# Optimization experiments

Hardware: AMD Instinct MI355X
Metric: run time of the kernel (lower is better)

## Reference

```python
import jax, jax.numpy as jnp
import numpy as np

B, S, DIM = 2, 2048, 2048
N_HEADS = 16
KV_LORA = 512
NOPE_D = 128
ROPE_D = 64
V_D = 128
Q_D = NOPE_D + ROPE_D  # 192
EPS = 1e-6


def _make_rope_cache(seqlen, head_dim):
    # [cos | sin] layout per position, GPT-NeoX half-rotation convention
    half = head_dim // 2
    inv_freq = 1.0 / (10000.0 ** (np.arange(0, half, dtype=np.float32) / half))
    t = np.arange(seqlen, dtype=np.float32)
    freqs = np.outer(t, inv_freq)                    # [S, half]
    emb = np.concatenate([freqs, freqs], axis=-1)    # [S, head_dim]
    return jnp.asarray(np.concatenate([np.cos(emb), np.sin(emb)], axis=-1))  # [S, 2*head_dim]


def setup_inputs() -> dict:
    key = jax.random.key(0)
    ks = jax.random.split(key, 6)
    x = jax.random.normal(ks[0], (B, S, DIM), dtype=jnp.float32)
    rope_cache = _make_rope_cache(S, ROPE_D)         # [S, 128]
    std = 0.02
    wq = jax.random.normal(ks[1], (N_HEADS * Q_D, DIM), dtype=jnp.float32) * std
    wkva = jax.random.normal(ks[2], (KV_LORA + ROPE_D, DIM), dtype=jnp.float32) * std
    norm_w = jnp.ones((KV_LORA,), dtype=jnp.float32)
    wkvb = jax.random.normal(ks[3], (N_HEADS * (NOPE_D + V_D), KV_LORA), dtype=jnp.float32) * std
    wo = jax.random.normal(ks[4], (DIM, N_HEADS * V_D), dtype=jnp.float32) * std
    return {"x": x, "rope_cache": rope_cache, "wq": wq, "wkva": wkva,
            "norm_w": norm_w, "wkvb": wkvb, "wo": wo}


def _rotate_half(t):
    h = t.shape[-1] // 2
    return jnp.concatenate([-t[..., h:], t[..., :h]], axis=-1)


def _rms_norm(t, w):
    tf = t.astype(jnp.float32)
    y = tf * jax.lax.rsqrt(jnp.mean(tf * tf, axis=-1, keepdims=True) + EPS)
    return (y * w).astype(t.dtype)


def reference(x, rope_cache, wq, wkva, norm_w, wkvb, wo):
    bs, seqlen, _ = x.shape
    scale = Q_D ** (-0.5)

    q = (x @ wq.T).reshape(bs, seqlen, N_HEADS, Q_D)
    q_nope, q_rope = q[..., :NOPE_D], q[..., NOPE_D:]

    ckv = x @ wkva.T                                 # [b,s,KV_LORA+ROPE_D]
    kv_pass, k_rope = ckv[..., :KV_LORA], ckv[..., KV_LORA:]
    kv = (_rms_norm(kv_pass, norm_w) @ wkvb.T).reshape(bs, seqlen, N_HEADS, NOPE_D + V_D)
    k_nope, v = kv[..., :NOPE_D], kv[..., NOPE_D:]

    k_rope = jnp.broadcast_to(k_rope[:, :, None, :], (bs, seqlen, N_HEADS, ROPE_D))

    cos = rope_cache[:seqlen, :ROPE_D][None, :, None, :]
    sin = rope_cache[:seqlen, ROPE_D:2 * ROPE_D][None, :, None, :]
    q_rope = q_rope * cos + _rotate_half(q_rope) * sin
    k_rope = k_rope * cos + _rotate_half(k_rope) * sin

    qf = jnp.concatenate([q_nope, q_rope], axis=-1)  # [b,s,h,192]
    kf = jnp.concatenate([k_nope, k_rope], axis=-1)

    # causal SDPA
    scores = jnp.einsum('bqhd,bkhd->bhqk', qf, kf) * scale
    mask = jnp.tril(jnp.ones((seqlen, seqlen), dtype=bool))
    scores = jnp.where(mask, scores, jnp.finfo(scores.dtype).min)
    probs = jax.nn.softmax(scores, axis=-1)
    out = jnp.einsum('bhqk,bkhd->bqhd', probs, v).reshape(bs, seqlen, N_HEADS * V_D)
    return out @ wo.T
```

## Files before the change

kernel.cpp:

```cpp
#include <hip/hip_runtime.h>
#include <cstdint>
#include <cstddef>

#define B_      2
#define S_      2048
#define DIM_    2048
#define H_      16
#define KV_LORA_ 512
#define NOPE_D_ 128
#define ROPE_D_ 64
#define V_D_    128
#define Q_D_    192
#define EPS_    1e-6f
#define BS_     (B_ * S_)
#define CKV_P_  768

typedef __attribute__((ext_vector_type(8))) short bf16x8;
typedef __attribute__((ext_vector_type(4))) float f32x4;
typedef __attribute__((ext_vector_type(16))) float f32x16;

__device__ __forceinline__ ushort f2bf(float f) {
    union { float f; uint32_t u; } v; v.f = f;
    uint32_t u = v.u + 0x7fff + ((v.u >> 16) & 1);
    return (ushort)(u >> 16);
}
__device__ __forceinline__ float bf2f(ushort u) {
    union { uint32_t u; float f; } v; v.u = (uint32_t)u << 16; return v.f;
}
__device__ __forceinline__ void gll16(const void* g, void* l) {
    __builtin_amdgcn_global_load_lds(
        (const __attribute__((address_space(1))) unsigned int*)g,
        (__attribute__((address_space(3))) unsigned int*)l, 16, 0, 0);
}

#define GQ_BARRIER()  __builtin_amdgcn_s_barrier()
#define GQ_LGKM0()    do { asm volatile("s_waitcnt lgkmcnt(0)" ::: "memory"); \
                           __builtin_amdgcn_sched_barrier(0); } while (0)

template <int MODE>
__global__ __launch_bounds__(512, 2) void gemm256_8ph(
    const ushort* __restrict__ A, const ushort* __restrict__ Bw,
    void* __restrict__ Cv, void* __restrict__ Cv2, int N, int K, int nbx)
{
    __shared__ __align__(16) ushort L[2][2][2][8192];

    const int tid = threadIdx.x;
    const int lane = tid & 63;
    const int w = tid >> 6;
    const int l15 = lane & 15, quad = lane >> 4;
    const int q8 = quad * 8;
    const int rsw8 = ((l15 >> 1) & 3) * 8;

    const int nwg = (int)gridDim.x;
    const int cpx = nwg >> 3;
    const int lin = (int)blockIdx.x;
    const int swz = (lin & 7) * cpx + (lin >> 3);
    const int m0 = (swz / nbx) * 256;
    const int n0 = (swz % nbx) * 256;

    const int wm0 = (w & 3) * 64;
    const int wn0 = (w >> 2) * 128;

    const int NT = K >> 6;

    f32x4 acc[4][8];
#pragma unroll
    for (int i = 0; i < 4; ++i)
#pragma unroll
        for (int j = 0; j < 8; ++j) acc[i][j] = (f32x4){0.f, 0.f, 0.f, 0.f};

    const int srow = lane >> 2;
    const int scg  = (lane & 3) ^ ((lane >> 3) & 3);

    auto stage = [&](int ab, int kh, int kt, int buf) {
#pragma unroll
        for (int j = 0; j < 2; ++j) {
            int ci = w + j * 8;
            ushort* dst = &L[buf][ab][kh][ci * 512 + lane * 8];
            int row = ci * 16 + srow;
            const ushort* src = (ab ? Bw + (size_t)(n0 + row) * K
                                    : A  + (size_t)(m0 + row) * K)
                                + kt * 64 + kh * 32 + scg * 8;
            gll16(src, dst);
        }
    };

    stage(0, 0, 0, 0); stage(1, 0, 0, 0); stage(0, 1, 0, 0); stage(1, 1, 0, 0);
    if (NT > 1) { stage(0, 0, 1, 1); stage(1, 0, 1, 1); stage(0, 1, 1, 1); }
    else        { stage(0, 0, 0, 1); stage(1, 0, 0, 1); stage(0, 1, 0, 1); }
    asm volatile("s_waitcnt vmcnt(6)" ::: "memory");
    GQ_BARRIER();

    bf16x8 a[4], b[4];

    for (int t = 0; t < NT; ++t) {
        const int c = t & 1, o = c ^ 1;
        const int kt1 = (t + 1 < NT) ? t + 1 : 0;
        const int kt2 = (t + 2 < NT) ? t + 2 : 0;

#pragma unroll
        for (int fm = 0; fm < 4; ++fm)
            a[fm] = *(const bf16x8*)&L[c][0][0][(wm0 + fm * 16 + l15) * 32 + (q8 ^ rsw8)];
#pragma unroll
        for (int fn = 0; fn < 4; ++fn)
            b[fn] = *(const bf16x8*)&L[c][1][0][(wn0 + fn * 16 + l15) * 32 + (q8 ^ rsw8)];
        stage(1, 1, kt1, o);
        GQ_BARRIER();
        GQ_LGKM0();
        __builtin_amdgcn_s_setprio(1);
#pragma unroll
        for (int fm = 0; fm < 4; ++fm)
#pragma unroll
            for (int fn = 0; fn < 4; ++fn)
                acc[fm][fn] = __builtin_amdgcn_mfma_f32_16x16x32_bf16(a[fm], b[fn], acc[fm][fn], 0, 0, 0);
        __builtin_amdgcn_s_setprio(0);
        GQ_BARRIER();

#pragma unroll
        for (int fn = 0; fn < 4; ++fn)
            b[fn] = *(const bf16x8*)&L[c][1][0][(wn0 + 64 + fn * 16 + l15) * 32 + (q8 ^ rsw8)];
        stage(0, 0, kt2, c);
        GQ_BARRIER();
        GQ_LGKM0();
        __builtin_amdgcn_s_setprio(1);
#pragma unroll
        for (int fm = 0; fm < 4; ++fm)
#pragma unroll
            for (int fn = 0; fn < 4; ++fn)
                acc[fm][4 + fn] = __builtin_amdgcn_mfma_f32_16x16x32_bf16(a[fm], b[fn], acc[fm][4 + fn], 0, 0, 0);
        __builtin_amdgcn_s_setprio(0);
        GQ_BARRIER();

#pragma unroll
        for (int fm = 0; fm < 4; ++fm)
            a[fm] = *(const bf16x8*)&L[c][0][1][(wm0 + fm * 16 + l15) * 32 + (q8 ^ rsw8)];
#pragma unroll
        for (int fn = 0; fn < 4; ++fn)
            b[fn] = *(const bf16x8*)&L[c][1][1][(wn0 + fn * 16 + l15) * 32 + (q8 ^ rsw8)];
        stage(1, 0, kt2, c);
        GQ_BARRIER();
        GQ_LGKM0();
        __builtin_amdgcn_s_setprio(1);
#pragma unroll
        for (int fm = 0; fm < 4; ++fm)
#pragma unroll
            for (int fn = 0; fn < 4; ++fn)
                acc[fm][fn] = __builtin_amdgcn_mfma_f32_16x16x32_bf16(a[fm], b[fn], acc[fm][fn], 0, 0, 0);
        __builtin_amdgcn_s_setprio(0);
        GQ_BARRIER();

#pragma unroll
        for (int fn = 0; fn < 4; ++fn)
            b[fn] = *(const bf16x8*)&L[c][1][1][(wn0 + 64 + fn * 16 + l15) * 32 + (q8 ^ rsw8)];
        stage(0, 1, kt2, c);
        GQ_BARRIER();
        GQ_LGKM0();
        __builtin_amdgcn_s_setprio(1);
#pragma unroll
        for (int fm = 0; fm < 4; ++fm)
#pragma unroll
            for (int fn = 0; fn < 4; ++fn)
                acc[fm][4 + fn] = __builtin_amdgcn_mfma_f32_16x16x32_bf16(a[fm], b[fn], acc[fm][4 + fn], 0, 0, 0);
        __builtin_amdgcn_s_setprio(0);
        asm volatile("s_waitcnt vmcnt(6)" ::: "memory");
        GQ_BARRIER();
    }

    if (MODE == 3) {
        asm volatile("s_waitcnt vmcnt(0)" ::: "memory");
        GQ_BARRIER();
        const int h = n0 >> 8;
        if (w < 4) {
#pragma unroll
            for (int fm = 0; fm < 4; ++fm)
#pragma unroll
                for (int r = 0; r < 4; ++r) {
                    size_t base = (size_t)(m0 + wm0 + fm * 16 + quad * 4 + r) * 4096
                                  + n0 + wn0 + l15;
#pragma unroll
                    for (int fn = 0; fn < 8; ++fn)
                        ((ushort*)Cv)[base + fn * 16] = f2bf(acc[fm][fn][r]);
                }
        } else {
            ushort* T = &L[0][0][0][0] + (size_t)(w - 4) * (128 * 80);
#pragma unroll
            for (int fm = 0; fm < 4; ++fm)
#pragma unroll
                for (int fn = 0; fn < 8; ++fn) {
                    uint32_t lo = (uint32_t)f2bf(acc[fm][fn][0])
                                | ((uint32_t)f2bf(acc[fm][fn][1]) << 16);
                    uint32_t hi2 = (uint32_t)f2bf(acc[fm][fn][2])
                                 | ((uint32_t)f2bf(acc[fm][fn][3]) << 16);
                    uint2 pk; pk.x = lo; pk.y = hi2;
                    *(uint2*)&T[(size_t)(fn * 16 + l15) * 80 + fm * 16 + quad * 4] = pk;
                }
            asm volatile("s_waitcnt lgkmcnt(0)" ::: "memory");
            __builtin_amdgcn_sched_barrier(0);
            const int bh = (m0 >> 11) * 16 + h;
            const int sbase = (m0 & 2047) + (w & 3) * 64;
            ushort* vT = (ushort*)Cv2;
#pragma unroll
            for (int j = 0; j < 16; ++j) {
                int cc = j * 64 + lane;
                int vd = cc >> 3;
                int s8 = (cc & 7) * 8;
                bf16x8 v = *(const bf16x8*)&T[(size_t)vd * 80 + s8];
                *(bf16x8*)(vT + ((size_t)bh * 128 + vd) * 2048 + sbase + s8) = v;
            }
        }
        return;
    }
#pragma unroll
    for (int fm = 0; fm < 4; ++fm)
#pragma unroll
        for (int r = 0; r < 4; ++r) {
            int row = m0 + wm0 + fm * 16 + quad * 4 + r;
            if (MODE == 2) {
                if (n0 < 3072) {
                    size_t base = (size_t)row * 3072 + n0 + wn0 + l15;
#pragma unroll
                    for (int fn = 0; fn < 8; ++fn)
                        ((ushort*)Cv)[base + fn * 16] = f2bf(acc[fm][fn][r]);
                } else {
                    size_t base = (size_t)row * CKV_P_ + (n0 - 3072) + wn0 + l15;
#pragma unroll
                    for (int fn = 0; fn < 8; ++fn)
                        ((float*)Cv2)[base + fn * 16] = acc[fm][fn][r];
                }
            } else {
                size_t base = (size_t)row * N + n0 + wn0 + l15;
#pragma unroll
                for (int fn = 0; fn < 8; ++fn) {
                    float v = acc[fm][fn][r];
                    if (MODE == 1) ((ushort*)Cv)[base + fn * 16] = f2bf(v);
                    else           ((float*)Cv)[base + fn * 16] = v;
                }
            }
        }
}

template <int OUT_BF16>
__global__ __launch_bounds__(512, 2) void gemm_bn128(
    const ushort* __restrict__ A, const ushort* __restrict__ Bw,
    void* __restrict__ Cv, int N, int K, int nbx)
{
    __shared__ __align__(16) ushort LA[2][2][4][256][8];
    __shared__ __align__(16) ushort LB[2][2][4][128][8];

    const int tid = threadIdx.x;
    const int lane = tid & 63;
    const int w = tid >> 6;
    const int l15 = lane & 15, quad = lane >> 4;

    const int nwg = (int)gridDim.x;
    const int cpx = nwg >> 3;
    const int lin = (int)blockIdx.x;
    const int swz = (lin & 7) * cpx + (lin >> 3);
    const int m0 = (swz / nbx) * 256;
    const int n0 = (swz % nbx) * 128;

    const int wm0 = (w & 3) * 64;
    const int wn0 = (w >> 2) * 64;

    const int NT = K >> 6;

    f32x4 acc[4][4];
#pragma unroll
    for (int i = 0; i < 4; ++i)
#pragma unroll
        for (int j = 0; j < 4; ++j) acc[i][j] = (f32x4){0.f, 0.f, 0.f, 0.f};

    auto stageA = [&](int kh, int kt, int buf) {
#pragma unroll
        for (int j = 0; j < 2; ++j) {
            int ci = w + j * 8;
            int qd = ci >> 2, rg = ci & 3;
            ushort* dst = &LA[buf][kh][qd][rg * 64 + lane][0];
            const ushort* src = A + (size_t)(m0 + rg * 64 + lane) * K
                                + kt * 64 + kh * 32 + qd * 8;
            gll16(src, dst);
        }
    };
    auto stageB = [&](int kt, int buf) {
#pragma unroll
        for (int j = 0; j < 2; ++j) {
            int ci = w + j * 8;
            int kh = ci >> 3, qd = (ci >> 1) & 3, rh = ci & 1;
            ushort* dst = &LB[buf][kh][qd][rh * 64 + lane][0];
            const ushort* src = Bw + (size_t)(n0 + rh * 64 + lane) * K
                                + kt * 64 + kh * 32 + qd * 8;
            gll16(src, dst);
        }
    };

    stageA(0, 0, 0); stageA(1, 0, 0); stageB(0, 0);
    stageA(0, (NT > 1) ? 1 : 0, 1);
    asm volatile("s_waitcnt vmcnt(2)" ::: "memory");
    GQ_BARRIER();

    bf16x8 a[4], b[4];

    for (int t = 0; t < NT; ++t) {
        const int c = t & 1, o = c ^ 1;
        const int kt1 = (t + 1 < NT) ? t + 1 : 0;
        const int kt2 = (t + 2 < NT) ? t + 2 : 0;

#pragma unroll
        for (int fm = 0; fm < 4; ++fm)
            a[fm] = *(const bf16x8*)&LA[c][0][quad][wm0 + fm * 16 + l15][0];
#pragma unroll
        for (int fn = 0; fn < 4; ++fn)
            b[fn] = *(const bf16x8*)&LB[c][0][quad][wn0 + fn * 16 + l15][0];
        stageA(1, kt1, o); stageB(kt1, o);
        GQ_BARRIER();
        GQ_LGKM0();
        __builtin_amdgcn_s_setprio(1);
#pragma unroll
        for (int fm = 0; fm < 4; ++fm)
#pragma unroll
            for (int fn = 0; fn < 4; ++fn)
                acc[fm][fn] = __builtin_amdgcn_mfma_f32_16x16x32_bf16(a[fm], b[fn], acc[fm][fn], 0, 0, 0);
        __builtin_amdgcn_s_setprio(0);
        GQ_BARRIER();

#pragma unroll
        for (int fm = 0; fm < 4; ++fm)
            a[fm] = *(const bf16x8*)&LA[c][1][quad][wm0 + fm * 16 + l15][0];
#pragma unroll
        for (int fn = 0; fn < 4; ++fn)
            b[fn] = *(const bf16x8*)&LB[c][1][quad][wn0 + fn * 16 + l15][0];
        stageA(0, kt2, c);
        GQ_BARRIER();
        GQ_LGKM0();
        __builtin_amdgcn_s_setprio(1);
#pragma unroll
        for (int fm = 0; fm < 4; ++fm)
#pragma unroll
            for (int fn = 0; fn < 4; ++fn)
                acc[fm][fn] = __builtin_amdgcn_mfma_f32_16x16x32_bf16(a[fm], b[fn], acc[fm][fn], 0, 0, 0);
        __builtin_amdgcn_s_setprio(0);
        asm volatile("s_waitcnt vmcnt(2)" ::: "memory");
        GQ_BARRIER();
    }

#pragma unroll
    for (int fm = 0; fm < 4; ++fm)
#pragma unroll
        for (int r = 0; r < 4; ++r) {
            size_t base = (size_t)(m0 + wm0 + fm * 16 + quad * 4 + r) * N + n0 + wn0 + l15;
#pragma unroll
            for (int fn = 0; fn < 4; ++fn) {
                float v = acc[fm][fn][r];
                if (OUT_BF16) ((ushort*)Cv)[base + fn * 16] = f2bf(v);
                else          ((float*)Cv)[base + fn * 16] = v;
            }
        }
}

__global__ __launch_bounds__(256) void cast_all(
    const float* __restrict__ x, const float* __restrict__ wq,
    const float* __restrict__ wkva, const float* __restrict__ wkvb,
    const float* __restrict__ wo,
    ushort* __restrict__ xb, ushort* __restrict__ wc,
    ushort* __restrict__ wkvb_bf, ushort* __restrict__ wo_bf)
{
    size_t i = ((size_t)blockIdx.x * 256 + threadIdx.x) * 8;
    const float* s; ushort* d;
    if (i < 8388608)        { s = x + i;                  d = xb + i; }
    else if (i < 14680064)  { s = wq + (i - 8388608);     d = wc + (i - 8388608); }
    else if (i < 15859712)  { s = wkva + (i - 14680064);  d = wc + (i - 8388608); }
    else if (i < 16252928)  {
        ushort4 z = {0, 0, 0, 0};
        ushort* dz = wc + (i - 8388608);
        *(ushort4*)dz = z; *(ushort4*)(dz + 4) = z;
        return;
    }
    else if (i < 18350080)  { s = wkvb + (i - 16252928);  d = wkvb_bf + (i - 16252928); }
    else                    { s = wo + (i - 18350080);    d = wo_bf + (i - 18350080); }
    float4 a = *(const float4*)s;
    float4 b = *(const float4*)(s + 4);
    ushort4 o0, o1;
    o0.x = f2bf(a.x); o0.y = f2bf(a.y); o0.z = f2bf(a.z); o0.w = f2bf(a.w);
    o1.x = f2bf(b.x); o1.y = f2bf(b.y); o1.z = f2bf(b.z); o1.w = f2bf(b.w);
    *(ushort4*)d = o0;
    *(ushort4*)(d + 4) = o1;
}

__global__ __launch_bounds__(256) void rmsnorm_rope_k(
    const float* __restrict__ ckv, const float* __restrict__ nw,
    const float* __restrict__ rope_cache,
    ushort* __restrict__ cnorm, ushort* __restrict__ krb)
{
    const int lane = threadIdx.x & 63;
    const int row = blockIdx.x * 4 + (threadIdx.x >> 6);
    const float* src = ckv + (size_t)row * CKV_P_;
    float4 a = *(const float4*)(src + lane * 4);
    float4 b = *(const float4*)(src + 256 + lane * 4);
    float ss = a.x*a.x + a.y*a.y + a.z*a.z + a.w*a.w
             + b.x*b.x + b.y*b.y + b.z*b.z + b.w*b.w;
#pragma unroll
    for (int off = 32; off > 0; off >>= 1) ss += __shfl_xor(ss, off, 64);
    float rs = rsqrtf(ss * (1.0f / 512.0f) + EPS_);
    float4 w0 = *(const float4*)(nw + lane * 4);
    float4 w1 = *(const float4*)(nw + 256 + lane * 4);
    ushort* dst = cnorm + (size_t)row * KV_LORA_;
    ushort4 o0, o1;
    o0.x = f2bf(a.x*rs*w0.x); o0.y = f2bf(a.y*rs*w0.y);
    o0.z = f2bf(a.z*rs*w0.z); o0.w = f2bf(a.w*rs*w0.w);
    o1.x = f2bf(b.x*rs*w1.x); o1.y = f2bf(b.y*rs*w1.y);
    o1.z = f2bf(b.z*rs*w1.z); o1.w = f2bf(b.w*rs*w1.w);
    *(ushort4*)(dst + lane * 4) = o0;
    *(ushort4*)(dst + 256 + lane * 4) = o1;

    float v = src[KV_LORA_ + lane];
    float other = __shfl_xor(v, 32, 64);
    float rot = (lane < 32) ? -other : other;
    int s = row & (S_ - 1);
    float c  = rope_cache[s * (2 * ROPE_D_) + lane];
    float sn = rope_cache[s * (2 * ROPE_D_) + ROPE_D_ + lane];
    krb[(size_t)row * ROPE_D_ + lane] = f2bf(v * c + rot * sn);
}

__global__ __launch_bounds__(512, 2) void mla_attn_mfma6(
    const ushort* __restrict__ qb, const ushort* __restrict__ kvb,
    const ushort* __restrict__ krb, const ushort* __restrict__ vT,
    const float* __restrict__ rope_cache, ushort* __restrict__ attn)
{
    __shared__ __align__(16) ushort LDSU[40960];
    const int KFo[2] = {0, 12288};
    const int VFo[2] = {24576, 32768};

    const int tid = threadIdx.x;
    const int lane = tid & 63;
    const int w = tid >> 6;
    const int l31 = lane & 31, hi = lane >> 5;
    const int band = w & 3;
    const int koff = (w >> 2) * 32;

    const int lin = (int)blockIdx.y * 8 + (int)blockIdx.x;
    const int swz = (lin & 7) * 32 + (lin >> 3);
    const int bh = swz >> 3;
    const int px = swz & 7;
    const int b = bh >> 4, h = bh & 15;
    const size_t bS = (size_t)b * S_;
    const float scale = 0.07216878364870323f;

    auto stage = [&](int kbase, int bufi) {
#pragma unroll
        for (int r = 0; r < 3; ++r) {
            int c = w + r * 8;
            ushort* dst = &LDSU[KFo[bufi] + (c * 64 + lane) * 8];
            const ushort* src = (c < 16)
                ? kvb + (bS + kbase + lane) * 4096 + h * 256 + c * 8
                : krb + (bS + kbase + lane) * 64 + (c - 16) * 8;
            gll16(src, dst);
        }
#pragma unroll
        for (int r = 0; r < 2; ++r) {
            int c = w + r * 8;
            ushort* dst = &LDSU[VFo[bufi] + (((c & 7) * 128) + (c >> 3) * 64 + lane) * 8];
            const ushort* src =
                vT + ((size_t)bh * 128 + (c >> 3) * 64 + lane) * S_ + kbase + (c & 7) * 8;
            gll16(src, dst);
        }
    };

#pragma unroll 1
    for (int hv = 0; hv < 2; ++hv) {
        const int qt = hv ? 15 - px : px;
        const int qbase = qt * 128;
        const int nkt = 2 * qt + 2;
        const int bmin = qbase + band * 32;

        stage(0, 0);

        bf16x8 qf[12];
        {
            const ushort* qrow = qb + (bS + bmin + l31) * (size_t)(H_ * Q_D_) + h * Q_D_;
#pragma unroll
            for (int c = 0; c < 8; ++c)
                qf[c] = *(const bf16x8*)(qrow + c * 16 + hi * 8);
            bf16x8 q8  = *(const bf16x8*)(qrow + 128 + hi * 8);
            bf16x8 q9  = *(const bf16x8*)(qrow + 144 + hi * 8);
            bf16x8 q10 = *(const bf16x8*)(qrow + 160 + hi * 8);
            bf16x8 q11 = *(const bf16x8*)(qrow + 176 + hi * 8);
            const float* rc = rope_cache + (size_t)(bmin + l31) * 128 + hi * 8;
            f32x4 c8a = *(const f32x4*)(rc + 0),  c8b = *(const f32x4*)(rc + 4);
            f32x4 c9a = *(const f32x4*)(rc + 16), c9b = *(const f32x4*)(rc + 20);
            f32x4 cAa = *(const f32x4*)(rc + 32), cAb = *(const f32x4*)(rc + 36);
            f32x4 cBa = *(const f32x4*)(rc + 48), cBb = *(const f32x4*)(rc + 52);
            f32x4 s8a = *(const f32x4*)(rc + 64), s8b = *(const f32x4*)(rc + 68);
            f32x4 s9a = *(const f32x4*)(rc + 80), s9b = *(const f32x4*)(rc + 84);
            f32x4 sAa = *(const f32x4*)(rc + 96), sAb = *(const f32x4*)(rc + 100);
            f32x4 sBa = *(const f32x4*)(rc + 112), sBb = *(const f32x4*)(rc + 116);
            bf16x8 o8, o9, o10, o11;
#pragma unroll
            for (int e = 0; e < 4; ++e) {
                float a8 = bf2f((ushort)q8[e]),  b8 = bf2f((ushort)q8[e + 4]);
                float a9 = bf2f((ushort)q9[e]),  b9 = bf2f((ushort)q9[e + 4]);
                float aA = bf2f((ushort)q10[e]), bA = bf2f((ushort)q10[e + 4]);
                float aB = bf2f((ushort)q11[e]), bB = bf2f((ushort)q11[e + 4]);
                o8[e]      = (short)f2bf(a8 * c8a[e] - aA * s8a[e]);
                o8[e + 4]  = (short)f2bf(b8 * c8b[e] - bA * s8b[e]);
                o9[e]      = (short)f2bf(a9 * c9a[e] - aB * s9a[e]);
                o9[e + 4]  = (short)f2bf(b9 * c9b[e] - bB * s9b[e]);
                o10[e]     = (short)f2bf(aA * cAa[e] + a8 * sAa[e]);
                o10[e + 4] = (short)f2bf(bA * cAb[e] + b8 * sAb[e]);
                o11[e]     = (short)f2bf(aB * cBa[e] + a9 * sBa[e]);
                o11[e + 4] = (short)f2bf(bB * cBb[e] + b9 * sBb[e]);
            }
            qf[8] = o8; qf[9] = o9; qf[10] = o10; qf[11] = o11;
        }

        f32x16 ov[4];
#pragma unroll
        for (int vt = 0; vt < 4; ++vt)
#pragma unroll
            for (int r = 0; r < 16; ++r) ov[vt][r] = 0.f;
        float m_run = -3e38f, lsum = 0.f;

        __syncthreads();

        for (int kt = 0; kt < nkt; ++kt) {
            const int kb = kt * 64;
            const int cur = kt & 1;
            if (kt + 1 < nkt) stage((kt + 1) * 64, cur ^ 1);

            const int kg = kb + koff;
            if (kg <= bmin + 31) {
                f32x16 sc;
#pragma unroll
                for (int r = 0; r < 16; ++r) sc[r] = 0.f;
                __builtin_amdgcn_s_setprio(1);
#pragma unroll
                for (int c = 0; c < 12; ++c) {
                    bf16x8 kf = *(const bf16x8*)
                        &LDSU[KFo[cur] + ((c * 2 + hi) * 64 + koff + l31) * 8];
                    sc = __builtin_amdgcn_mfma_f32_32x32x16_bf16(kf, qf[c], sc, 0, 0, 0);
                }
                __builtin_amdgcn_s_setprio(0);

                const bool need_mask = (kg == bmin);
                float p[16]; float mx = -3e38f;
#pragma unroll
                for (int r = 0; r < 16; ++r) {
                    float v = sc[r] * scale;
                    if (need_mask) {
                        int kr = (r & 3) + 8 * (r >> 2) + 4 * hi;
                        if (kr > l31) v = -3e38f;
                    }
                    p[r] = v; mx = fmaxf(mx, v);
                }
                mx = fmaxf(mx, __shfl_xor(mx, 32, 64));
                if (!__all(mx - m_run <= 8.0f)) {
                    float mn = fmaxf(mx, m_run);
                    float al = __expf(m_run - mn);
                    m_run = mn; lsum *= al;
#pragma unroll
                    for (int vt = 0; vt < 4; ++vt)
#pragma unroll
                        for (int r = 0; r < 16; ++r) ov[vt][r] *= al;
                }
                float s_loc = 0.f;
#pragma unroll
                for (int r = 0; r < 16; ++r) { p[r] = __expf(p[r] - m_run); s_loc += p[r]; }
                lsum += s_loc + __shfl_xor(s_loc, 32, 64);

                uint32_t w8[8];
#pragma unroll
                for (int m = 0; m < 8; ++m)
                    w8[m] = (uint32_t)f2bf(p[2 * m]) | ((uint32_t)f2bf(p[2 * m + 1]) << 16);
                bf16x8 pb[2];
#pragma unroll
                for (int c = 0; c < 2; ++c) {
                    uint32_t wd[4];
#pragma unroll
                    for (int par = 0; par < 2; ++par) {
                        uint32_t a  = w8[4 * c + par];
                        uint32_t bb = w8[4 * c + 2 + par];
                        uint32_t t  = __shfl_xor(bb, 32, 64);
                        uint32_t t2 = __shfl_xor(a, 32, 64);
                        wd[par]     = hi ? t : a;
                        wd[par + 2] = hi ? bb : t2;
                    }
                    union { uint32_t u[4]; bf16x8 v; } cvt;
                    cvt.u[0] = wd[0]; cvt.u[1] = wd[1]; cvt.u[2] = wd[2]; cvt.u[3] = wd[3];
                    pb[c] = cvt.v;
                }

                __builtin_amdgcn_s_setprio(1);
#pragma unroll
                for (int vt = 0; vt < 4; ++vt)
#pragma unroll
                    for (int c = 0; c < 2; ++c) {
                        bf16x8 vf = *(const bf16x8*)
                            &LDSU[VFo[cur] + (((koff >> 3) + c * 2 + hi) * 128 + vt * 32 + l31) * 8];
                        ov[vt] = __builtin_amdgcn_mfma_f32_32x32x16_bf16(vf, pb[c], ov[vt], 0, 0, 0);
                    }
                __builtin_amdgcn_s_setprio(0);
            }
            __syncthreads();
        }

        float* mrg = (float*)LDSU;
        if (w >= 4) {
            float* dst = mrg + (size_t)((w - 4) * 64 + lane) * 68;
#pragma unroll
            for (int vt = 0; vt < 4; ++vt)
#pragma unroll
                for (int g = 0; g < 4; ++g) {
                    f32x4 v4v = { ov[vt][g * 4 + 0], ov[vt][g * 4 + 1],
                                  ov[vt][g * 4 + 2], ov[vt][g * 4 + 3] };
                    *(f32x4*)(dst + vt * 16 + g * 4) = v4v;
                }
            dst[64] = m_run; dst[65] = lsum;
        }
        __syncthreads();
        if (w < 4) {
            const float* srcm = mrg + (size_t)(w * 64 + lane) * 68;
            float mB = srcm[64], lB = srcm[65];
            float M = fmaxf(m_run, mB);
            float eA = __expf(m_run - M), eB = __expf(mB - M);
            float L = lsum * eA + lB * eB;
            float inv = 1.0f / L;
            size_t obase = (bS + bmin + l31) * (size_t)(H_ * V_D_) + h * V_D_;
#pragma unroll
            for (int vt = 0; vt < 4; ++vt)
#pragma unroll
                for (int g = 0; g < 4; ++g) {
                    ushort4 o;
                    o.x = f2bf((ov[vt][g*4+0] * eA + srcm[vt*16+g*4+0] * eB) * inv);
                    o.y = f2bf((ov[vt][g*4+1] * eA + srcm[vt*16+g*4+1] * eB) * inv);
                    o.z = f2bf((ov[vt][g*4+2] * eA + srcm[vt*16+g*4+2] * eB) * inv);
                    o.w = f2bf((ov[vt][g*4+3] * eA + srcm[vt*16+g*4+3] * eB) * inv);
                    *(ushort4*)(attn + obase + vt * 32 + g * 8 + hi * 4) = o;
                }
        }
        __syncthreads();
    }
}

extern "C" void kernel_launch(void* const* d_in, const int* in_sizes, int n_in,
                              void* d_out, int out_size, void* d_ws, size_t ws_size,
                              hipStream_t stream)
{
    const float* x          = (const float*)d_in[0];
    const float* rope_cache = (const float*)d_in[1];
    const float* wq         = (const float*)d_in[2];
    const float* wkva       = (const float*)d_in[3];
    const float* norm_w     = (const float*)d_in[4];
    const float* wkvb       = (const float*)d_in[5];
    const float* wo         = (const float*)d_in[6];
    float* out = (float*)d_out;

    char* p = (char*)d_ws;
    ushort* xb       = (ushort*)p; p += (size_t)BS_ * DIM_ * 2;
    ushort* q_bf     = (ushort*)p; p += (size_t)BS_ * H_ * Q_D_ * 2;
    float*  ckv      = (float*) p; p += (size_t)BS_ * CKV_P_ * 4;
    ushort* cnorm_bf = (ushort*)p; p += (size_t)BS_ * KV_LORA_ * 2;
    ushort* kvb      = (ushort*)p; p += (size_t)BS_ * 4096 * 2;
    ushort* attn_bf  = (ushort*)p; p += (size_t)BS_ * 2048 * 2;
    ushort* krb      = (ushort*)p; p += (size_t)BS_ * ROPE_D_ * 2;
    ushort* wc_bf    = (ushort*)p; p += (size_t)3840 * DIM_ * 2;
    ushort* wkvb_bf  = (ushort*)p; p += (size_t)4096 * KV_LORA_ * 2;
    ushort* wo_bf    = (ushort*)p; p += (size_t)DIM_ * 2048 * 2;
    ushort* vT       = xb;

    cast_all<<<11008, dim3(256), 0, stream>>>(
        x, wq, wkva, wkvb, wo, xb, wc_bf, wkvb_bf, wo_bf);

    gemm256_8ph<2><<<dim3(16 * 15), dim3(512), 0, stream>>>(
        xb, wc_bf, q_bf, ckv, 0, DIM_, 15);
    rmsnorm_rope_k<<<BS_ / 4, dim3(256), 0, stream>>>(
        ckv, norm_w, rope_cache, cnorm_bf, krb);
    gemm256_8ph<3><<<dim3(16 * 16), dim3(512), 0, stream>>>(
        cnorm_bf, wkvb_bf, kvb, vT, 4096, KV_LORA_, 16);
    mla_attn_mfma6<<<dim3(8, B_ * H_), dim3(512), 0, stream>>>(
        q_bf, kvb, krb, vT, rope_cache, attn_bf);
    gemm_bn128<0><<<dim3(16 * 16), dim3(512), 0, stream>>>(
        attn_bf, wo_bf, out, 2048, 2048, 16);
}
```

Before: 362.3 us.

## Use row-major XOR-swizzled LDS tiles in output GEMM and attention kernel

Both the output-projection GEMM and the attention kernel stop using a column-chunk-major LDS layout and switch to row-major tiles whose 16-byte chunks are XOR-swizzled by row. Each lane of the global-to-LDS copy now loads consecutive 16-byte chunks within a row, which makes global reads more contiguous. Reads from LDS apply the matching swizzle so bank conflicts stay low. In exchange there is extra index arithmetic, and any mismatch between the store and load swizzles would produce wrong results.

New measurement: 340.7 us. 6.0% less time.

```diff
diff --git a/kernel.cpp b/kernel.cpp
--- a/kernel.cpp
+++ b/kernel.cpp
@@ -244,13 +244,15 @@
     const ushort* __restrict__ A, const ushort* __restrict__ Bw,
     void* __restrict__ Cv, int N, int K, int nbx)
 {
-    __shared__ __align__(16) ushort LA[2][2][4][256][8];
-    __shared__ __align__(16) ushort LB[2][2][4][128][8];
+    __shared__ __align__(16) ushort LA[2][2][8192];
+    __shared__ __align__(16) ushort LB[2][2][4096];
 
     const int tid = threadIdx.x;
     const int lane = tid & 63;
     const int w = tid >> 6;
     const int l15 = lane & 15, quad = lane >> 4;
+    const int q8 = quad * 8;
+    const int rsw8 = ((l15 >> 1) & 3) * 8;
 
     const int nwg = (int)gridDim.x;
     const int cpx = nwg >> 3;
@@ -270,25 +272,27 @@
 #pragma unroll
         for (int j = 0; j < 4; ++j) acc[i][j] = (f32x4){0.f, 0.f, 0.f, 0.f};
 
+    const int srow = lane >> 2;
+    const int scg  = (lane & 3) ^ ((lane >> 3) & 3);
+
     auto stageA = [&](int kh, int kt, int buf) {
 #pragma unroll
         for (int j = 0; j < 2; ++j) {
             int ci = w + j * 8;
-            int qd = ci >> 2, rg = ci & 3;
-            ushort* dst = &LA[buf][kh][qd][rg * 64 + lane][0];
-            const ushort* src = A + (size_t)(m0 + rg * 64 + lane) * K
-                                + kt * 64 + kh * 32 + qd * 8;
+            ushort* dst = &LA[buf][kh][ci * 512 + lane * 8];
+            int row = ci * 16 + srow;
+            const ushort* src = A + (size_t)(m0 + row) * K
+                                + kt * 64 + kh * 32 + scg * 8;
             gll16(src, dst);
         }
     };
     auto stageB = [&](int kt, int buf) {
 #pragma unroll
         for (int j = 0; j < 2; ++j) {
-            int ci = w + j * 8;
-            int kh = ci >> 3, qd = (ci >> 1) & 3, rh = ci & 1;
-            ushort* dst = &LB[buf][kh][qd][rh * 64 + lane][0];
-            const ushort* src = Bw + (size_t)(n0 + rh * 64 + lane) * K
-                                + kt * 64 + kh * 32 + qd * 8;
+            ushort* dst = &LB[buf][j][(w * 64 + lane) * 8];
+            int row = w * 16 + srow;
+            const ushort* src = Bw + (size_t)(n0 + row) * K
+                                + kt * 64 + j * 32 + scg * 8;
             gll16(src, dst);
         }
     };
@@ -307,10 +311,10 @@
 
 #pragma unroll
         for (int fm = 0; fm < 4; ++fm)
-            a[fm] = *(const bf16x8*)&LA[c][0][quad][wm0 + fm * 16 + l15][0];
+            a[fm] = *(const bf16x8*)&LA[c][0][(wm0 + fm * 16 + l15) * 32 + (q8 ^ rsw8)];
 #pragma unroll
         for (int fn = 0; fn < 4; ++fn)
-            b[fn] = *(const bf16x8*)&LB[c][0][quad][wn0 + fn * 16 + l15][0];
+            b[fn] = *(const bf16x8*)&LB[c][0][(wn0 + fn * 16 + l15) * 32 + (q8 ^ rsw8)];
         stageA(1, kt1, o); stageB(kt1, o);
         GQ_BARRIER();
         GQ_LGKM0();
@@ -325,10 +329,10 @@
 
 #pragma unroll
         for (int fm = 0; fm < 4; ++fm)
-            a[fm] = *(const bf16x8*)&LA[c][1][quad][wm0 + fm * 16 + l15][0];
+            a[fm] = *(const bf16x8*)&LA[c][1][(wm0 + fm * 16 + l15) * 32 + (q8 ^ rsw8)];
 #pragma unroll
         for (int fn = 0; fn < 4; ++fn)
-            b[fn] = *(const bf16x8*)&LB[c][1][quad][wn0 + fn * 16 + l15][0];
+            b[fn] = *(const bf16x8*)&LB[c][1][(wn0 + fn * 16 + l15) * 32 + (q8 ^ rsw8)];
         stageA(0, kt2, c);
         GQ_BARRIER();
         GQ_LGKM0();
@@ -421,14 +425,15 @@
     krb[(size_t)row * ROPE_D_ + lane] = f2bf(v * c + rot * sn);
 }
 
-__global__ __launch_bounds__(512, 2) void mla_attn_mfma6(
+__global__ __launch_bounds__(512, 2) void mla_attn_mfma7(
     const ushort* __restrict__ qb, const ushort* __restrict__ kvb,
     const ushort* __restrict__ krb, const ushort* __restrict__ vT,
     const float* __restrict__ rope_cache, ushort* __restrict__ attn)
 {
     __shared__ __align__(16) ushort LDSU[40960];
-    const int KFo[2] = {0, 12288};
-    const int VFo[2] = {24576, 32768};
+    const int KNo[2] = {0, 8192};
+    const int KRo[2] = {16384, 20480};
+    const int VVo[2] = {24576, 32768};
 
     const int tid = threadIdx.x;
     const int lane = tid & 63;
@@ -447,20 +452,29 @@
 
     auto stage = [&](int kbase, int bufi) {
 #pragma unroll
-        for (int r = 0; r < 3; ++r) {
-            int c = w + r * 8;
-            ushort* dst = &LDSU[KFo[bufi] + (c * 64 + lane) * 8];
-            const ushort* src = (c < 16)
-                ? kvb + (bS + kbase + lane) * 4096 + h * 256 + c * 8
-                : krb + (bS + kbase + lane) * 64 + (c - 16) * 8;
+        for (int j = 0; j < 2; ++j) {
+            int g = (j * 8 + w) * 64 + lane;
+            int row = g >> 4;
+            int d8 = (g & 15) ^ (row & 7);
+            ushort* dst = &LDSU[KNo[bufi] + g * 8];
+            const ushort* src = kvb + (bS + kbase + row) * 4096 + h * 256 + d8 * 8;
             gll16(src, dst);
         }
-#pragma unroll
-        for (int r = 0; r < 2; ++r) {
-            int c = w + r * 8;
-            ushort* dst = &LDSU[VFo[bufi] + (((c & 7) * 128) + (c >> 3) * 64 + lane) * 8];
-            const ushort* src =
-                vT + ((size_t)bh * 128 + (c >> 3) * 64 + lane) * S_ + kbase + (c & 7) * 8;
+        {
+            int g = w * 64 + lane;
+            int row = g >> 3;
+            int r8 = (g & 7) ^ (row & 7);
+            ushort* dst = &LDSU[KRo[bufi] + g * 8];
+            const ushort* src = krb + (bS + kbase + row) * 64 + r8 * 8;
+            gll16(src, dst);
+        }
+#pragma unroll
+        for (int j = 0; j < 2; ++j) {
+            int g = (j * 8 + w) * 64 + lane;
+            int vd = g >> 3;
+            int kc = (g & 7) ^ (vd & 7);
+            ushort* dst = &LDSU[VVo[bufi] + g * 8];
+            const ushort* src = vT + ((size_t)bh * 128 + vd) * 2048 + kbase + kc * 8;
             gll16(src, dst);
         }
     };
@@ -521,6 +535,10 @@
 
         __syncthreads();
 
+        const int krow = koff + l31;
+        const int kx7 = krow & 7;
+        const int vx7 = l31 & 7;
+
         for (int kt = 0; kt < nkt; ++kt) {
             const int kb = kt * 64;
             const int cur = kt & 1;
@@ -534,9 +552,12 @@
                 __builtin_amdgcn_s_setprio(1);
 #pragma unroll
                 for (int c = 0; c < 12; ++c) {
-                    bf16x8 kf = *(const bf16x8*)
-                        &LDSU[KFo[cur] + ((c * 2 + hi) * 64 + koff + l31) * 8];
-                    sc = __builtin_amdgcn_mfma_f32_32x32x16_bf16(kf, qf[c], sc, 0, 0, 0);
+                    const bf16x8* kp;
+                    if (c < 8)
+                        kp = (const bf16x8*)&LDSU[KNo[cur] + (krow * 16 + ((c * 2 + hi) ^ kx7)) * 8];
+                    else
+                        kp = (const bf16x8*)&LDSU[KRo[cur] + (krow * 8 + (((c - 8) * 2 + hi) ^ kx7)) * 8];
+                    sc = __builtin_amdgcn_mfma_f32_32x32x16_bf16(*kp, qf[c], sc, 0, 0, 0);
                 }
                 __builtin_amdgcn_s_setprio(0);
 
@@ -592,10 +613,12 @@
 #pragma unroll
                 for (int vt = 0; vt < 4; ++vt)
 #pragma unroll
-                    for (int c = 0; c < 2; ++c) {
+                    for (int cc = 0; cc < 2; ++cc) {
+                        int vd = vt * 32 + l31;
+                        int k8 = (koff >> 3) + cc * 2 + hi;
                         bf16x8 vf = *(const bf16x8*)
-                            &LDSU[VFo[cur] + (((koff >> 3) + c * 2 + hi) * 128 + vt * 32 + l31) * 8];
-                        ov[vt] = __builtin_amdgcn_mfma_f32_32x32x16_bf16(vf, pb[c], ov[vt], 0, 0, 0);
+                            &LDSU[VVo[cur] + (vd * 8 + (k8 ^ vx7)) * 8];
+                        ov[vt] = __builtin_amdgcn_mfma_f32_32x32x16_bf16(vf, pb[cc], ov[vt], 0, 0, 0);
                     }
                 __builtin_amdgcn_s_setprio(0);
             }
@@ -675,7 +698,7 @@
         ckv, norm_w, rope_cache, cnorm_bf, krb);
     gemm256_8ph<3><<<dim3(16 * 16), dim3(512), 0, stream>>>(
         cnorm_bf, wkvb_bf, kvb, vT, 4096, KV_LORA_, 16);
-    mla_attn_mfma6<<<dim3(8, B_ * H_), dim3(512), 0, stream>>>(
+    mla_attn_mfma7<<<dim3(8, B_ * H_), dim3(512), 0, stream>>>(
         q_bf, kvb, krb, vT, rope_cache, attn_bf);
     gemm_bn128<0><<<dim3(16 * 16), dim3(512), 0, stream>>>(
         attn_bf, wo_bf, out, 2048, 2048, 16);
```
